# Kernel optimization log

Hardware: AMD Instinct MI355X
Metric: run time of the kernel (lower is better)

The kernel has to match this reference:

```python
import jax, jax.numpy as jnp
import numpy as np

TARGET_SCALE = 0.06  # normalize_scale / embedding_scale when normalize=True


def setup_inputs() -> dict:
    key = jax.random.key(0)
    k1, k2 = jax.random.split(key)
    N, S, C, V, K = 8, 2048, 4, 128, 512
    x0 = jax.random.normal(k1, (N, S, C, V), dtype=jnp.float32)
    # embedding init: randn * embedding_scale (after_update renorm is redundant
    # under normalize=True since forward re-normalizes rows anyway)
    embedding0 = jax.random.normal(k2, (C, K, V), dtype=jnp.float32) * TARGET_SCALE
    return {"x0": x0, "embedding0": embedding0}


def reference(x0, embedding0):
    N, S, C, V = x0.shape
    K = embedding0.shape[1]
    target_norm = TARGET_SCALE * jnp.sqrt(jnp.asarray(V, jnp.float32))

    # normalize inputs and codebook rows to target_norm (p=2 over vec_len)
    x = target_norm * x0 / jnp.linalg.norm(x0, axis=3, keepdims=True)            # [N,S,C,V]
    emb = target_norm * embedding0 / jnp.linalg.norm(embedding0, axis=2, keepdims=True)  # [C,K,V]

    # nearest code per (n,s,c): argmin ||x - e||, computed via the expansion
    # ||x||^2 + ||e||^2 - 2<x,e> (same argmin, avoids [N*S,C,K,V] diff tensor)
    x2 = jnp.sum(x * x, axis=3)                    # [N,S,C]
    e2 = jnp.sum(emb * emb, axis=2)                # [C,K]
    xe = jnp.einsum('nscv,ckv->nsck', x, emb)      # [N,S,C,K]
    d2 = x2[..., None] + e2[None, None] - 2.0 * xe
    index = jnp.argmin(d2, axis=3)                 # [N,S,C] int

    # entropy of code usage: histc over ALL indices, normalized by N*S (torch len(index))
    hist = jnp.zeros((K,), jnp.float32).at[index.reshape(-1)].add(1.0)
    prob = hist / jnp.float32(N * S)
    entropy = -jnp.sum(jnp.where(hist > 0, prob * jnp.log(jnp.where(hist > 0, prob, 1.0)), 0.0))
    entropy = jax.lax.stop_gradient(entropy)

    # gather codebook vectors: output[n,s,c] = emb[c, index[n,s,c]]
    output = emb[jnp.arange(C)[None, None, :], index]  # [N,S,C,V]

    # straight-through
    discrete = x + jax.lax.stop_gradient(output - x)

    vq_pen = jnp.sum((jax.lax.stop_gradient(x) - output) ** 2, axis=3)           # [N,S,C]
    encoder_pen = (jnp.sum((x - jax.lax.stop_gradient(output)) ** 2, axis=3)
                   + jnp.sum((x - x0) ** 2, axis=3))                              # [N,S,C]

    offset = jnp.arange(C, dtype=index.dtype) * K
    index1 = index + offset[None, None, :]                                        # [N,S,C]

    return (discrete, index1, vq_pen, encoder_pen, entropy)
```

## Files before the change

kernel.cpp:

```cpp
#include <hip/hip_runtime.h>
#include <math.h>

#define TARGET_SCALE 0.06f
constexpr int N_ = 8, S_ = 2048, C_ = 4, V_ = 128, K_ = 512;
constexpr int NS = N_ * S_;
constexpr int NQ = NS * C_;

constexpr int O_DISC = 0;
constexpr int O_IDX  = NQ * V_;
constexpr int O_VQ   = O_IDX + NQ;
constexpr int O_ENC  = O_VQ + NQ;
constexpr int O_ENT  = O_ENC + NQ;

constexpr int WS_EMB  = 0;
constexpr int WS_E2   = C_ * K_ * V_;
constexpr int WS_HIST = WS_E2 + C_ * K_;

constexpr int QB  = 64;
constexpr int KC  = 64;
constexpr int XSP = 132;
constexpr int ESP = 68;

__global__ __launch_bounds__(256) void prep_emb(const float* __restrict__ emb0,
                                                float* __restrict__ ws) {
    const int wave = threadIdx.x >> 6;
    const int lane = threadIdx.x & 63;
    const int row  = blockIdx.x * 4 + wave;
    const float tn = TARGET_SCALE * sqrtf((float)V_);

    float2 e = *(const float2*)(emb0 + row * V_ + lane * 2);
    float ss = e.x * e.x + e.y * e.y;
    #pragma unroll
    for (int off = 32; off; off >>= 1) ss += __shfl_xor(ss, off);
    const float nrm = sqrtf(ss);

    float2 en;
    en.x = (tn * e.x) / nrm;
    en.y = (tn * e.y) / nrm;
    *(float2*)(ws + WS_EMB + row * V_ + lane * 2) = en;

    float s2 = en.x * en.x + en.y * en.y;
    #pragma unroll
    for (int off = 32; off; off >>= 1) s2 += __shfl_xor(s2, off);
    if (lane == 0) ws[WS_E2 + row] = s2;

    if (blockIdx.x == 0) {
        ws[WS_HIST + threadIdx.x]       = 0.f;
        ws[WS_HIST + 256 + threadIdx.x] = 0.f;
    }
}

__global__ __launch_bounds__(256) void vq_main(const float* __restrict__ x0,
                                               float* __restrict__ ws,
                                               float* __restrict__ out) {
    __shared__ float XS[QB * XSP];
    __shared__ float ES[KC * ESP];
    __shared__ float s_scale[QB];
    __shared__ float s_x2[QB];
    __shared__ float s_es2[KC];
    __shared__ int   s_bestk[QB];

    const int c   = blockIdx.y;
    const int tid = threadIdx.x;
    const int qg  = tid >> 4;
    const int kg  = tid & 15;
    const float tn = TARGET_SCALE * sqrtf((float)V_);

    const float* __restrict__ embc = ws + WS_EMB + c * K_ * V_;
    const float* __restrict__ e2c  = ws + WS_E2 + c * K_;
    float* __restrict__ hist = ws + WS_HIST;

    for (int tile = blockIdx.x; tile < NS / QB; tile += gridDim.x) {
        const int nsBase = tile * QB;

        __syncthreads();
        #pragma unroll
        for (int it = 0; it < 8; ++it) {
            int fi  = tid + 256 * it;
            int row = fi >> 5, u4 = fi & 31;
            float4 v = *(const float4*)(x0 + ((nsBase + row) * C_ + c) * V_ + u4 * 4);
            *(float4*)(XS + row * XSP + u4 * 4) = v;
        }
        __syncthreads();

        {
            const int row = tid >> 2, j = tid & 3;
            const float4* xr4 = (const float4*)(XS + row * XSP + j * 32);
            float ss = 0.f;
            #pragma unroll
            for (int m = 0; m < 8; ++m) {
                float4 v = xr4[m];
                ss += v.x * v.x + v.y * v.y + v.z * v.z + v.w * v.w;
            }
            ss += __shfl_xor(ss, 1);
            ss += __shfl_xor(ss, 2);
            const float scale = tn / sqrtf(ss);
            float x2 = 0.f;
            #pragma unroll
            for (int m = 0; m < 8; ++m) {
                float4 v = xr4[m];
                float a = scale * v.x, b = scale * v.y, d = scale * v.z, e = scale * v.w;
                x2 += a * a + b * b + d * d + e * e;
            }
            x2 += __shfl_xor(x2, 1);
            x2 += __shfl_xor(x2, 2);
            if (j == 0) { s_scale[row] = scale; s_x2[row] = x2; }
        }
        __syncthreads();

        float bd[4]; int bk[4];
        #pragma unroll
        for (int qq = 0; qq < 4; ++qq) { bd[qq] = 3.4e38f; bk[qq] = 0x7fffffff; }

        for (int kc = 0; kc < K_ / KC; ++kc) {
            float acc[4][4] = {{0.f}};
            for (int vh = 0; vh < 2; ++vh) {
                __syncthreads();
                #pragma unroll
                for (int it = 0; it < 4; ++it) {
                    int fi = tid + 256 * it;
                    int r = fi >> 4, u4 = fi & 15;
                    float4 v = *(const float4*)(embc + (kc * KC + r) * V_ + vh * 64 + u4 * 4);
                    *(float4*)(ES + r * ESP + u4 * 4) = v;
                }
                if (vh == 0 && tid < KC) s_es2[tid] = e2c[kc * KC + tid];
                __syncthreads();

                #pragma unroll
                for (int vq = 0; vq < 16; ++vq) {
                    float4 xv[4], ev[4];
                    #pragma unroll
                    for (int qq = 0; qq < 4; ++qq)
                        xv[qq] = *(const float4*)(XS + (qg + 16 * qq) * XSP + vh * 64 + vq * 4);
                    #pragma unroll
                    for (int kk = 0; kk < 4; ++kk)
                        ev[kk] = *(const float4*)(ES + (kg + 16 * kk) * ESP + vq * 4);
                    #pragma unroll
                    for (int qq = 0; qq < 4; ++qq)
                        #pragma unroll
                        for (int kk = 0; kk < 4; ++kk) {
                            acc[qq][kk] = fmaf(xv[qq].x, ev[kk].x, acc[qq][kk]);
                            acc[qq][kk] = fmaf(xv[qq].y, ev[kk].y, acc[qq][kk]);
                            acc[qq][kk] = fmaf(xv[qq].z, ev[kk].z, acc[qq][kk]);
                            acc[qq][kk] = fmaf(xv[qq].w, ev[kk].w, acc[qq][kk]);
                        }
                }
            }
            #pragma unroll
            for (int kk = 0; kk < 4; ++kk) {
                const int kloc  = kg + 16 * kk;
                const float e2v = s_es2[kloc];
                const int kglob = kc * KC + kloc;
                #pragma unroll
                for (int qq = 0; qq < 4; ++qq) {
                    const int ql = qg + 16 * qq;
                    const float xe = s_scale[ql] * acc[qq][kk];
                    const float t  = s_x2[ql] + e2v;
                    const float d  = fmaf(-2.f, xe, t);
                    if (d < bd[qq]) { bd[qq] = d; bk[qq] = kglob; }
                }
            }
        }

        #pragma unroll
        for (int off = 8; off; off >>= 1) {
            #pragma unroll
            for (int qq = 0; qq < 4; ++qq) {
                float od = __shfl_xor(bd[qq], off);
                int   ok = __shfl_xor(bk[qq], off);
                if (od < bd[qq] || (od == bd[qq] && ok < bk[qq])) { bd[qq] = od; bk[qq] = ok; }
            }
        }
        if (kg == 0) {
            #pragma unroll
            for (int qq = 0; qq < 4; ++qq) s_bestk[qg + 16 * qq] = bk[qq];
        }
        __syncthreads();

        {
            const int q = tid >> 2, j = tid & 3;
            const int kstar   = s_bestk[q];
            const float scale = s_scale[q];
            const int qglob   = (nsBase + q) * C_ + c;
            const float* er = embc + kstar * V_ + j * 32;
            const float* xr = XS + q * XSP + j * 32;
            float* dr = out + O_DISC + qglob * V_ + j * 32;
            float vqp = 0.f, en2 = 0.f;
            #pragma unroll
            for (int m = 0; m < 8; ++m) {
                float4 e4 = *(const float4*)(er + m * 4);
                float4 x4 = *(const float4*)(xr + m * 4);
                float xa = scale * x4.x, xb = scale * x4.y, xc = scale * x4.z, xd = scale * x4.w;
                float da = xa - e4.x, db = xb - e4.y, dc = xc - e4.z, dd = xd - e4.w;
                vqp += da * da + db * db + dc * dc + dd * dd;
                float ga = xa - x4.x, gb = xb - x4.y, gc = xc - x4.z, gd = xd - x4.w;
                en2 += ga * ga + gb * gb + gc * gc + gd * gd;
                *(float4*)(dr + m * 4) = e4;
            }
            vqp += __shfl_xor(vqp, 1);
            vqp += __shfl_xor(vqp, 2);
            en2 += __shfl_xor(en2, 1);
            en2 += __shfl_xor(en2, 2);
            if (j == 0) {
                out[O_IDX + qglob] = (float)(kstar + c * K_);
                out[O_VQ  + qglob] = vqp;
                out[O_ENC + qglob] = vqp + en2;
                atomicAdd(hist + kstar, 1.0f);
            }
        }
    }
}

__global__ __launch_bounds__(256) void entropy_k(const float* __restrict__ ws,
                                                 float* __restrict__ out) {
    const float* hist = ws + WS_HIST;
    const int t = threadIdx.x;
    float s = 0.f;
    for (int i = t; i < K_; i += 256) {
        float h = hist[i];
        if (h > 0.f) {
            float p = h / (float)NQ;
            s += p * logf(p);
        }
    }
    #pragma unroll
    for (int off = 32; off; off >>= 1) s += __shfl_xor(s, off);
    __shared__ float wsum[4];
    if ((t & 63) == 0) wsum[t >> 6] = s;
    __syncthreads();
    if (t == 0) out[O_ENT] = -(wsum[0] + wsum[1] + wsum[2] + wsum[3]);
}

extern "C" void kernel_launch(void* const* d_in, const int* in_sizes, int n_in,
                              void* d_out, int out_size, void* d_ws, size_t ws_size,
                              hipStream_t stream) {
    const float* x0   = (const float*)d_in[0];
    const float* emb0 = (const float*)d_in[1];
    float* out = (float*)d_out;
    float* ws  = (float*)d_ws;

    prep_emb<<<512, 256, 0, stream>>>(emb0, ws);
    vq_main<<<dim3(128, 4), 256, 0, stream>>>(x0, ws, out);
    entropy_k<<<1, 256, 0, stream>>>(ws, out);
}
```

Measured before the change: 248.3 us.

## Retile VQ distance kernel to 8x4 register tile with V-chunked LDS staging

```diff
diff --git a/kernel.cpp b/kernel.cpp
--- a/kernel.cpp
+++ b/kernel.cpp
@@ -17,9 +17,9 @@
 constexpr int WS_HIST = WS_E2 + C_ * K_;
 
 constexpr int QB  = 64;
-constexpr int KC  = 64;
-constexpr int XSP = 132;
-constexpr int ESP = 68;
+constexpr int KCH = 128;
+constexpr int VCH = 32;
+constexpr int LSP = 36;
 
 __global__ __launch_bounds__(256) void prep_emb(const float* __restrict__ emb0,
                                                 float* __restrict__ ws) {
@@ -50,163 +50,161 @@
     }
 }
 
-__global__ __launch_bounds__(256) void vq_main(const float* __restrict__ x0,
-                                               float* __restrict__ ws,
-                                               float* __restrict__ out) {
-    __shared__ float XS[QB * XSP];
-    __shared__ float ES[KC * ESP];
+__global__ __launch_bounds__(256, 4) void vq_main(const float* __restrict__ x0,
+                                                  float* __restrict__ ws,
+                                                  float* __restrict__ out) {
+    __shared__ float ES[KCH * LSP];
+    __shared__ float XS[QB * LSP];
     __shared__ float s_scale[QB];
     __shared__ float s_x2[QB];
-    __shared__ float s_es2[KC];
+    __shared__ float s_es2[KCH];
     __shared__ int   s_bestk[QB];
 
-    const int c   = blockIdx.y;
-    const int tid = threadIdx.x;
-    const int qg  = tid >> 4;
-    const int kg  = tid & 15;
-    const float tn = TARGET_SCALE * sqrtf((float)V_);
+    const int c      = blockIdx.y;
+    const int tid    = threadIdx.x;
+    const int kg     = tid & 31;
+    const int qg     = tid >> 5;
+    const int nsBase = blockIdx.x * QB;
+    const float tn   = TARGET_SCALE * sqrtf((float)V_);
 
     const float* __restrict__ embc = ws + WS_EMB + c * K_ * V_;
     const float* __restrict__ e2c  = ws + WS_E2 + c * K_;
     float* __restrict__ hist = ws + WS_HIST;
 
-    for (int tile = blockIdx.x; tile < NS / QB; tile += gridDim.x) {
-        const int nsBase = tile * QB;
-
-        __syncthreads();
-        #pragma unroll
-        for (int it = 0; it < 8; ++it) {
-            int fi  = tid + 256 * it;
-            int row = fi >> 5, u4 = fi & 31;
-            float4 v = *(const float4*)(x0 + ((nsBase + row) * C_ + c) * V_ + u4 * 4);
-            *(float4*)(XS + row * XSP + u4 * 4) = v;
-        }
-        __syncthreads();
-
-        {
-            const int row = tid >> 2, j = tid & 3;
-            const float4* xr4 = (const float4*)(XS + row * XSP + j * 32);
-            float ss = 0.f;
-            #pragma unroll
-            for (int m = 0; m < 8; ++m) {
-                float4 v = xr4[m];
-                ss += v.x * v.x + v.y * v.y + v.z * v.z + v.w * v.w;
-            }
-            ss += __shfl_xor(ss, 1);
-            ss += __shfl_xor(ss, 2);
-            const float scale = tn / sqrtf(ss);
-            float x2 = 0.f;
-            #pragma unroll
-            for (int m = 0; m < 8; ++m) {
-                float4 v = xr4[m];
-                float a = scale * v.x, b = scale * v.y, d = scale * v.z, e = scale * v.w;
-                x2 += a * a + b * b + d * d + e * e;
-            }
-            x2 += __shfl_xor(x2, 1);
-            x2 += __shfl_xor(x2, 2);
-            if (j == 0) { s_scale[row] = scale; s_x2[row] = x2; }
-        }
-        __syncthreads();
-
-        float bd[4]; int bk[4];
-        #pragma unroll
-        for (int qq = 0; qq < 4; ++qq) { bd[qq] = 3.4e38f; bk[qq] = 0x7fffffff; }
-
-        for (int kc = 0; kc < K_ / KC; ++kc) {
-            float acc[4][4] = {{0.f}};
-            for (int vh = 0; vh < 2; ++vh) {
-                __syncthreads();
+    {
+        const int row = tid >> 2, j = tid & 3;
+        const float* xr = x0 + ((size_t)(nsBase + row) * C_ + c) * V_ + j * 32;
+        float ss = 0.f;
+        #pragma unroll
+        for (int m = 0; m < 8; ++m) {
+            float4 v = *(const float4*)(xr + m * 4);
+            ss += v.x * v.x + v.y * v.y + v.z * v.z + v.w * v.w;
+        }
+        ss += __shfl_xor(ss, 1);
+        ss += __shfl_xor(ss, 2);
+        const float scale = tn / sqrtf(ss);
+        float x2 = 0.f;
+        #pragma unroll
+        for (int m = 0; m < 8; ++m) {
+            float4 v = *(const float4*)(xr + m * 4);
+            float a = scale * v.x, b = scale * v.y, d = scale * v.z, e = scale * v.w;
+            x2 += a * a + b * b + d * d + e * e;
+        }
+        x2 += __shfl_xor(x2, 1);
+        x2 += __shfl_xor(x2, 2);
+        if (j == 0) { s_scale[row] = scale; s_x2[row] = x2; }
+    }
+
+    float bd[8]; int bk[8];
+    #pragma unroll
+    for (int qq = 0; qq < 8; ++qq) { bd[qq] = 3.4e38f; bk[qq] = 0x7fffffff; }
+
+    for (int kc = 0; kc < K_ / KCH; ++kc) {
+        float acc[8][4];
+        #pragma unroll
+        for (int qq = 0; qq < 8; ++qq)
+            #pragma unroll
+            for (int kk = 0; kk < 4; ++kk) acc[qq][kk] = 0.f;
+
+        for (int vc = 0; vc < V_ / VCH; ++vc) {
+            __syncthreads();
+            #pragma unroll
+            for (int it = 0; it < 4; ++it) {
+                int fi = tid + 256 * it;
+                int r = fi >> 3, slot = fi & 7;
+                float4 v = *(const float4*)(embc + (size_t)(kc * KCH + r) * V_ + vc * VCH + slot * 4);
+                *(float4*)(ES + r * LSP + slot * 4) = v;
+            }
+            #pragma unroll
+            for (int it = 0; it < 2; ++it) {
+                int fi = tid + 256 * it;
+                int r = fi >> 3, slot = fi & 7;
+                float4 v = *(const float4*)(x0 + ((size_t)(nsBase + r) * C_ + c) * V_ + vc * VCH + slot * 4);
+                *(float4*)(XS + r * LSP + slot * 4) = v;
+            }
+            if (vc == 0 && tid < KCH) s_es2[tid] = e2c[kc * KCH + tid];
+            __syncthreads();
+
+            #pragma unroll
+            for (int vq = 0; vq < 8; ++vq) {
+                float4 ev[4], xv[8];
                 #pragma unroll
-                for (int it = 0; it < 4; ++it) {
-                    int fi = tid + 256 * it;
-                    int r = fi >> 4, u4 = fi & 15;
-                    float4 v = *(const float4*)(embc + (kc * KC + r) * V_ + vh * 64 + u4 * 4);
-                    *(float4*)(ES + r * ESP + u4 * 4) = v;
-                }
-                if (vh == 0 && tid < KC) s_es2[tid] = e2c[kc * KC + tid];
-                __syncthreads();
-
+                for (int kk = 0; kk < 4; ++kk)
+                    ev[kk] = *(const float4*)(ES + (kg + 32 * kk) * LSP + vq * 4);
                 #pragma unroll
-                for (int vq = 0; vq < 16; ++vq) {
-                    float4 xv[4], ev[4];
+                for (int qq = 0; qq < 8; ++qq)
+                    xv[qq] = *(const float4*)(XS + (qg + 8 * qq) * LSP + vq * 4);
+                #pragma unroll
+                for (int qq = 0; qq < 8; ++qq)
                     #pragma unroll
-                    for (int qq = 0; qq < 4; ++qq)
-                        xv[qq] = *(const float4*)(XS + (qg + 16 * qq) * XSP + vh * 64 + vq * 4);
-                    #pragma unroll
-                    for (int kk = 0; kk < 4; ++kk)
-                        ev[kk] = *(const float4*)(ES + (kg + 16 * kk) * ESP + vq * 4);
-                    #pragma unroll
-                    for (int qq = 0; qq < 4; ++qq)
-                        #pragma unroll
-                        for (int kk = 0; kk < 4; ++kk) {
-                            acc[qq][kk] = fmaf(xv[qq].x, ev[kk].x, acc[qq][kk]);
-                            acc[qq][kk] = fmaf(xv[qq].y, ev[kk].y, acc[qq][kk]);
-                            acc[qq][kk] = fmaf(xv[qq].z, ev[kk].z, acc[qq][kk]);
-                            acc[qq][kk] = fmaf(xv[qq].w, ev[kk].w, acc[qq][kk]);
-                        }
-                }
-            }
-            #pragma unroll
-            for (int kk = 0; kk < 4; ++kk) {
-                const int kloc  = kg + 16 * kk;
-                const float e2v = s_es2[kloc];
-                const int kglob = kc * KC + kloc;
-                #pragma unroll
-                for (int qq = 0; qq < 4; ++qq) {
-                    const int ql = qg + 16 * qq;
-                    const float xe = s_scale[ql] * acc[qq][kk];
-                    const float t  = s_x2[ql] + e2v;
-                    const float d  = fmaf(-2.f, xe, t);
-                    if (d < bd[qq]) { bd[qq] = d; bk[qq] = kglob; }
-                }
-            }
-        }
-
-        #pragma unroll
-        for (int off = 8; off; off >>= 1) {
-            #pragma unroll
-            for (int qq = 0; qq < 4; ++qq) {
-                float od = __shfl_xor(bd[qq], off);
-                int   ok = __shfl_xor(bk[qq], off);
-                if (od < bd[qq] || (od == bd[qq] && ok < bk[qq])) { bd[qq] = od; bk[qq] = ok; }
-            }
-        }
-        if (kg == 0) {
-            #pragma unroll
-            for (int qq = 0; qq < 4; ++qq) s_bestk[qg + 16 * qq] = bk[qq];
-        }
-        __syncthreads();
-
-        {
-            const int q = tid >> 2, j = tid & 3;
-            const int kstar   = s_bestk[q];
-            const float scale = s_scale[q];
-            const int qglob   = (nsBase + q) * C_ + c;
-            const float* er = embc + kstar * V_ + j * 32;
-            const float* xr = XS + q * XSP + j * 32;
-            float* dr = out + O_DISC + qglob * V_ + j * 32;
-            float vqp = 0.f, en2 = 0.f;
-            #pragma unroll
-            for (int m = 0; m < 8; ++m) {
-                float4 e4 = *(const float4*)(er + m * 4);
-                float4 x4 = *(const float4*)(xr + m * 4);
-                float xa = scale * x4.x, xb = scale * x4.y, xc = scale * x4.z, xd = scale * x4.w;
-                float da = xa - e4.x, db = xb - e4.y, dc = xc - e4.z, dd = xd - e4.w;
-                vqp += da * da + db * db + dc * dc + dd * dd;
-                float ga = xa - x4.x, gb = xb - x4.y, gc = xc - x4.z, gd = xd - x4.w;
-                en2 += ga * ga + gb * gb + gc * gc + gd * gd;
-                *(float4*)(dr + m * 4) = e4;
-            }
-            vqp += __shfl_xor(vqp, 1);
-            vqp += __shfl_xor(vqp, 2);
-            en2 += __shfl_xor(en2, 1);
-            en2 += __shfl_xor(en2, 2);
-            if (j == 0) {
-                out[O_IDX + qglob] = (float)(kstar + c * K_);
-                out[O_VQ  + qglob] = vqp;
-                out[O_ENC + qglob] = vqp + en2;
-                atomicAdd(hist + kstar, 1.0f);
-            }
+                    for (int kk = 0; kk < 4; ++kk) {
+                        acc[qq][kk] = fmaf(xv[qq].x, ev[kk].x, acc[qq][kk]);
+                        acc[qq][kk] = fmaf(xv[qq].y, ev[kk].y, acc[qq][kk]);
+                        acc[qq][kk] = fmaf(xv[qq].z, ev[kk].z, acc[qq][kk]);
+                        acc[qq][kk] = fmaf(xv[qq].w, ev[kk].w, acc[qq][kk]);
+                    }
+            }
+        }
+
+        #pragma unroll
+        for (int kk = 0; kk < 4; ++kk) {
+            const int kloc  = kg + 32 * kk;
+            const float e2v = s_es2[kloc];
+            const int kglob = kc * KCH + kloc;
+            #pragma unroll
+            for (int qq = 0; qq < 8; ++qq) {
+                const int ql = qg + 8 * qq;
+                const float xe = s_scale[ql] * acc[qq][kk];
+                const float d  = fmaf(-2.f, xe, s_x2[ql] + e2v);
+                if (d < bd[qq]) { bd[qq] = d; bk[qq] = kglob; }
+            }
+        }
+    }
+
+    #pragma unroll
+    for (int off = 16; off; off >>= 1) {
+        #pragma unroll
+        for (int qq = 0; qq < 8; ++qq) {
+            float od = __shfl_xor(bd[qq], off);
+            int   ok = __shfl_xor(bk[qq], off);
+            if (od < bd[qq] || (od == bd[qq] && ok < bk[qq])) { bd[qq] = od; bk[qq] = ok; }
+        }
+    }
+    if (kg == 0) {
+        #pragma unroll
+        for (int qq = 0; qq < 8; ++qq) s_bestk[qg + 8 * qq] = bk[qq];
+    }
+    __syncthreads();
+
+    {
+        const int q = tid >> 2, j = tid & 3;
+        const int kstar   = s_bestk[q];
+        const float scale = s_scale[q];
+        const size_t qglob = (size_t)(nsBase + q) * C_ + c;
+        const float* er = embc + (size_t)kstar * V_ + j * 32;
+        const float* xr = x0 + qglob * V_ + j * 32;
+        float* dr = out + O_DISC + qglob * V_ + j * 32;
+        float vqp = 0.f, en2 = 0.f;
+        #pragma unroll
+        for (int m = 0; m < 8; ++m) {
+            float4 e4 = *(const float4*)(er + m * 4);
+            float4 x4 = *(const float4*)(xr + m * 4);
+            float xa = scale * x4.x, xb = scale * x4.y, xc = scale * x4.z, xd = scale * x4.w;
+            float da = xa - e4.x, db = xb - e4.y, dc = xc - e4.z, dd = xd - e4.w;
+            vqp += da * da + db * db + dc * dc + dd * dd;
+            float ga = xa - x4.x, gb = xb - x4.y, gc = xc - x4.z, gd = xd - x4.w;
+            en2 += ga * ga + gb * gb + gc * gc + gd * gd;
+            *(float4*)(dr + m * 4) = e4;
+        }
+        vqp += __shfl_xor(vqp, 1);
+        vqp += __shfl_xor(vqp, 2);
+        en2 += __shfl_xor(en2, 1);
+        en2 += __shfl_xor(en2, 2);
+        if (j == 0) {
+            out[O_IDX + qglob] = (float)(kstar + c * K_);
+            out[O_VQ  + qglob] = vqp;
+            out[O_ENC + qglob] = vqp + en2;
+            atomicAdd(hist + kstar, 1.0f);
         }
     }
 }
@@ -219,7 +217,7 @@
     for (int i = t; i < K_; i += 256) {
         float h = hist[i];
         if (h > 0.f) {
-            float p = h / (float)NQ;
+            float p = h / (float)NS;
             s += p * logf(p);
         }
     }
@@ -240,6 +238,6 @@
     float* ws  = (float*)d_ws;
 
     prep_emb<<<512, 256, 0, stream>>>(emb0, ws);
-    vq_main<<<dim3(128, 4), 256, 0, stream>>>(x0, ws, out);
+    vq_main<<<dim3(NS / QB, C_), 256, 0, stream>>>(x0, ws, out);
     entropy_k<<<1, 256, 0, stream>>>(ws, out);
 }
```

Measured after the change: 353.1 us. 42.2% more time.
